# Performance work log

Measured on AMD Instinct MI355X. Metric: run time of the kernel, lower is better.

The kernel has to match this reference:

```python
import jax, jax.numpy as jnp
import numpy as np

WH = 7          # window height
WW = 7          # window width
HEADS = 8
HEAD_DIM = 64   # inner_dim = heads * 64 hard-coded in module
SCALE = HEAD_DIM ** (-0.5)


def _relative_position_index():
    # identical construction to the torch module, done once in numpy
    coords = np.stack(np.meshgrid(np.arange(WH), np.arange(WW), indexing='ij'))  # [2,Wh,Ww]
    cf = coords.reshape(2, -1)                       # [2, Wh*Ww]
    rel = cf[:, :, None] - cf[:, None, :]            # [2, N, N]
    rel = rel.transpose(1, 2, 0).copy()              # [N, N, 2]
    rel[:, :, 0] += WH - 1
    rel[:, :, 1] += WW - 1
    rel[:, :, 0] *= 2 * WW - 1
    return rel.sum(-1)                               # [N, N] int

REL_IDX = jnp.asarray(_relative_position_index())


def setup_inputs() -> dict:
    key = jax.random.key(0)
    ks = jax.random.split(key, 4)
    B, C, H, W = 32, 384, 56, 56
    inner = HEADS * HEAD_DIM  # 512
    return {
        'x': jax.random.normal(ks[0], (B, C, H, W), jnp.float32),
        'w_qkv': jax.random.normal(ks[1], (C, 3 * inner), jnp.float32) * 0.02,
        'b_qkv': jnp.zeros((3 * inner,), jnp.float32),
        'w_out': jax.random.normal(ks[2], (inner, C), jnp.float32) * 0.02,
        'b_out': jnp.zeros((C,), jnp.float32),
        'bias_table': jax.random.normal(ks[3], ((2 * WH - 1) * (2 * WW - 1), HEADS), jnp.float32) * 0.01,
    }


def reference(x, w_qkv, b_qkv, w_out, b_out, bias_table):
    B, C, H, W = x.shape
    r1, r2 = H // WH, W // WW
    N = WH * WW  # 49 tokens per window
    # window partition: b c (r1 h1) (r2 w1) -> (b r1 r2) (h1 w1) c
    xw = x.reshape(B, C, r1, WH, r2, WW).transpose(0, 2, 4, 3, 5, 1)
    xw = xw.reshape(B * r1 * r2, N, C)
    # qkv projection
    qkv = xw @ w_qkv + b_qkv                                # [BM, N, 3*inner]
    q, k, v = jnp.split(qkv, 3, axis=2)
    q = q * SCALE
    def to_heads(t):
        BM = t.shape[0]
        return t.reshape(BM, N, HEADS, HEAD_DIM).transpose(0, 2, 1, 3)  # [BM,h,N,d]
    q, k, v = to_heads(q), to_heads(k), to_heads(v)
    attn = jnp.einsum('bhmc,bhnc->bhmn', q, k)              # [BM,h,N,N]
    # relative position bias gather
    bias = bias_table[REL_IDX.reshape(-1)].reshape(N, N, HEADS).transpose(2, 0, 1)
    attn = attn + bias[None]
    attn = jax.nn.softmax(attn, axis=3)
    out = jnp.einsum('bhmn,bhnc->bhmc', attn, v)            # [BM,h,N,d]
    out = out.transpose(0, 2, 1, 3).reshape(B * r1 * r2, N, HEADS * HEAD_DIM)
    out = out @ w_out + b_out                               # [BM,N,C]
    # reverse window partition: (b r1 r2) (h1 w1) c -> b c (r1 h1) (r2 w1)
    out = out.reshape(B, r1, r2, WH, WW, C).transpose(0, 5, 1, 3, 2, 4)
    out = out.reshape(B, C, H, W)
    return out, attn
```

## Files before the change

### kernel.cpp

```cpp
#include <hip/hip_runtime.h>

typedef __attribute__((ext_vector_type(8))) short s16x8;
typedef __attribute__((ext_vector_type(4))) short s16x4;
typedef __attribute__((ext_vector_type(4))) float f32x4;

#define NTOK 49
#define CDIM 384
#define INNER 512
#define XW_STRIDE 408
#define PL_STRIDE 88

__device__ __forceinline__ short f2bf(float f) {
  unsigned u = __float_as_uint(f);
  u += 0x7fffu + ((u >> 16) & 1u);
  return (short)(u >> 16);
}

__device__ __forceinline__ f32x4 mfma16(s16x8 a, s16x8 b, f32x4 c) {
  return __builtin_amdgcn_mfma_f32_16x16x32_bf16(a, b, c, 0, 0, 0);
}

__global__ void prep_kernel(const float* __restrict__ w_qkv, const float* __restrict__ w_out,
                            const float* __restrict__ bias_table,
                            short* __restrict__ wqkvT, short* __restrict__ woutT,
                            float* __restrict__ biasm) {
  int i = blockIdx.x * 256 + threadIdx.x;
  if (i < 1536 * CDIM) {
    int col = i % 1536, k = i / 1536;
    wqkvT[(size_t)col * CDIM + k] = f2bf(w_qkv[(size_t)k * 1536 + col]);
  } else if (i < 1536 * CDIM + CDIM * INNER) {
    int j = i - 1536 * CDIM;
    int c = j % CDIM, ii = j / CDIM;
    woutT[(size_t)c * INNER + ii] = f2bf(w_out[(size_t)ii * CDIM + c]);
  } else if (i < 1536 * CDIM + CDIM * INNER + 8 * NTOK * NTOK) {
    int j = i - 1536 * CDIM - CDIM * INNER;
    int h = j / 2401, t = j % 2401;
    int m = t / 49, n = t % 49;
    int rel = (m / 7 - n / 7 + 6) * 13 + (m % 7 - n % 7 + 6);
    biasm[j] = bias_table[rel * 8 + h];
  }
}

__global__ __launch_bounds__(512, 1) void qkv_kernel(
    const float* __restrict__ x, const float* __restrict__ b_qkv,
    const short* __restrict__ wqkvT,
    short* __restrict__ qs, short* __restrict__ ks, short* __restrict__ vs) {
  __shared__ short xw[64 * XW_STRIDE];
  const int win = blockIdx.x;
  const int b = win >> 6, r1 = (win >> 3) & 7, r2 = win & 7;
  const int tid = threadIdx.x;
  const float* xb = x + (size_t)b * CDIM * 3136 + (r1 * 7) * 56 + (r2 * 7);
  {
    const int mm = tid & 63;
    const int c0 = tid >> 6;
    int xoff = -1;
    if (mm < NTOK) xoff = (mm / 7) * 56 + (mm % 7);
    for (int it = 0; it < 48; ++it) {
      int c = c0 + it * 8;
      float v = (xoff >= 0) ? xb[(size_t)c * 3136 + xoff] : 0.f;
      xw[mm * XW_STRIDE + c] = f2bf(v);
    }
  }
  __syncthreads();
  const int wave = tid >> 6, lane = tid & 63;
  const int l15 = lane & 15, l4 = lane >> 4;
  const size_t hb = (size_t)win * 8 + wave;
  for (int tile = 0; tile < 3; ++tile) {
    f32x4 acc[4][4];
#pragma unroll
    for (int fm = 0; fm < 4; ++fm)
#pragma unroll
      for (int fn = 0; fn < 4; ++fn) acc[fm][fn] = (f32x4){0.f, 0.f, 0.f, 0.f};
    const short* wb = wqkvT + ((size_t)tile * 512 + wave * 64) * CDIM;
    for (int kk = 0; kk < 12; ++kk) {
      s16x8 av[4], bv[4];
#pragma unroll
      for (int fm = 0; fm < 4; ++fm)
        av[fm] = *(const s16x8*)(&xw[(fm * 16 + l15) * XW_STRIDE + kk * 32 + l4 * 8]);
#pragma unroll
      for (int fn = 0; fn < 4; ++fn)
        bv[fn] = *(const s16x8*)(wb + (size_t)(fn * 16 + l15) * CDIM + kk * 32 + l4 * 8);
#pragma unroll
      for (int fm = 0; fm < 4; ++fm)
#pragma unroll
        for (int fn = 0; fn < 4; ++fn)
          acc[fm][fn] = mfma16(av[fm], bv[fn], acc[fm][fn]);
    }
    float bq[4];
#pragma unroll
    for (int fn = 0; fn < 4; ++fn)
      bq[fn] = b_qkv[tile * 512 + wave * 64 + fn * 16 + l15];
    if (tile < 2) {
      short* dst = (tile == 0 ? qs : ks) + hb * (NTOK * 64);
      const float scl = (tile == 0) ? 0.125f : 1.f;
#pragma unroll
      for (int fm = 0; fm < 4; ++fm)
#pragma unroll
        for (int j = 0; j < 4; ++j) {
          int m = fm * 16 + l4 * 4 + j;
          if (m < NTOK) {
#pragma unroll
            for (int fn = 0; fn < 4; ++fn)
              dst[m * 64 + fn * 16 + l15] = f2bf((acc[fm][fn][j] + bq[fn]) * scl);
          }
        }
    } else {
      short* dst = vs + hb * 4096;
#pragma unroll
      for (int fm = 0; fm < 4; ++fm) {
        int bm = fm * 16 + l4 * 4;
#pragma unroll
        for (int fn = 0; fn < 4; ++fn) {
          int d = fn * 16 + l15;
          if (bm + 3 < NTOK) {
            s16x4 pk;
#pragma unroll
            for (int j = 0; j < 4; ++j) pk[j] = f2bf(acc[fm][fn][j] + bq[fn]);
            *(s16x4*)(dst + d * 64 + bm) = pk;
          } else if (bm < NTOK) {
#pragma unroll
            for (int j = 0; j < 4; ++j)
              if (bm + j < NTOK) dst[d * 64 + bm + j] = f2bf(acc[fm][fn][j] + bq[fn]);
          }
        }
      }
    }
  }
}

__global__ __launch_bounds__(64) void attn_kernel(
    const short* __restrict__ qs, const short* __restrict__ ks, const short* __restrict__ vs,
    const float* __restrict__ biasm, float* __restrict__ attn_out, short* __restrict__ os) {
  __shared__ short pl[64 * PL_STRIDE];
  const int blk = blockIdx.x;
  const int win = blk >> 3, h = blk & 7;
  const int lane = threadIdx.x;
  const int l15 = lane & 15, l4 = lane >> 4;
  const short* qb = qs + (size_t)blk * (NTOK * 64);
  const short* kb = ks + (size_t)blk * (NTOK * 64);
  f32x4 acc[4][4];
#pragma unroll
  for (int fm = 0; fm < 4; ++fm)
#pragma unroll
    for (int fn = 0; fn < 4; ++fn) acc[fm][fn] = (f32x4){0.f, 0.f, 0.f, 0.f};
#pragma unroll
  for (int kk = 0; kk < 2; ++kk) {
    s16x8 av[4], bv[4];
#pragma unroll
    for (int fm = 0; fm < 4; ++fm)
      av[fm] = *(const s16x8*)(qb + (fm * 16 + l15) * 64 + kk * 32 + l4 * 8);
#pragma unroll
    for (int fn = 0; fn < 4; ++fn)
      bv[fn] = *(const s16x8*)(kb + (fn * 16 + l15) * 64 + kk * 32 + l4 * 8);
#pragma unroll
    for (int fm = 0; fm < 4; ++fm)
#pragma unroll
      for (int fn = 0; fn < 4; ++fn)
        acc[fm][fn] = mfma16(av[fm], bv[fn], acc[fm][fn]);
  }
  const float* bh = biasm + h * 2401;
  float* ao = attn_out + (size_t)blk * (NTOK * NTOK);
#pragma unroll
  for (int fm = 0; fm < 4; ++fm) {
#pragma unroll
    for (int j = 0; j < 4; ++j) {
      const int m = fm * 16 + l4 * 4 + j;
      const bool mok = (m < NTOK);
      float sv[4], p[4];
#pragma unroll
      for (int fn = 0; fn < 4; ++fn) {
        int n = fn * 16 + l15;
        float bias = (mok && n < NTOK) ? bh[m * 49 + n] : 0.f;
        sv[fn] = acc[fm][fn][j] + bias;
      }
      float mx = -1e30f;
#pragma unroll
      for (int fn = 0; fn < 4; ++fn)
        if (fn * 16 + l15 < NTOK) mx = fmaxf(mx, sv[fn]);
      mx = fmaxf(mx, __shfl_xor(mx, 1));
      mx = fmaxf(mx, __shfl_xor(mx, 2));
      mx = fmaxf(mx, __shfl_xor(mx, 4));
      mx = fmaxf(mx, __shfl_xor(mx, 8));
      float sum = 0.f;
#pragma unroll
      for (int fn = 0; fn < 4; ++fn) {
        int n = fn * 16 + l15;
        p[fn] = (n < NTOK) ? __expf(sv[fn] - mx) : 0.f;
        sum += p[fn];
      }
      sum += __shfl_xor(sum, 1);
      sum += __shfl_xor(sum, 2);
      sum += __shfl_xor(sum, 4);
      sum += __shfl_xor(sum, 8);
      const float inv = 1.f / sum;
#pragma unroll
      for (int fn = 0; fn < 4; ++fn) {
        int n = fn * 16 + l15;
        float pv = p[fn] * inv;
        if (mok && n < NTOK) ao[m * 49 + n] = pv;
        pl[m * PL_STRIDE + n] = f2bf(pv);
      }
    }
  }
  __syncthreads();
  const short* vb = vs + (size_t)blk * 4096;
  f32x4 oacc[4][4];
#pragma unroll
  for (int fm = 0; fm < 4; ++fm)
#pragma unroll
    for (int fn = 0; fn < 4; ++fn) oacc[fm][fn] = (f32x4){0.f, 0.f, 0.f, 0.f};
#pragma unroll
  for (int kk = 0; kk < 2; ++kk) {
    s16x8 av[4], bv[4];
#pragma unroll
    for (int fm = 0; fm < 4; ++fm)
      av[fm] = *(const s16x8*)(&pl[(fm * 16 + l15) * PL_STRIDE + kk * 32 + l4 * 8]);
#pragma unroll
    for (int fn = 0; fn < 4; ++fn)
      bv[fn] = *(const s16x8*)(vb + (fn * 16 + l15) * 64 + kk * 32 + l4 * 8);
#pragma unroll
    for (int fm = 0; fm < 4; ++fm)
#pragma unroll
      for (int fn = 0; fn < 4; ++fn)
        oacc[fm][fn] = mfma16(av[fm], bv[fn], oacc[fm][fn]);
  }
  short* ob = os + (size_t)win * (NTOK * INNER) + h * 64;
#pragma unroll
  for (int fm = 0; fm < 4; ++fm)
#pragma unroll
    for (int j = 0; j < 4; ++j) {
      int m = fm * 16 + l4 * 4 + j;
      if (m < NTOK) {
#pragma unroll
        for (int fn = 0; fn < 4; ++fn)
          ob[m * INNER + fn * 16 + l15] = f2bf(oacc[fm][fn][j]);
      }
    }
}

__global__ __launch_bounds__(384, 1) void oproj_kernel(
    const short* __restrict__ os, const short* __restrict__ woutT,
    const float* __restrict__ b_out, float* __restrict__ outp) {
  __shared__ float ot[CDIM * 57];
  const int win = blockIdx.x;
  const int b = win >> 6, r1 = (win >> 3) & 7, r2 = win & 7;
  const int tid = threadIdx.x;
  const int wave = tid >> 6, lane = tid & 63;
  const int l15 = lane & 15, l4 = lane >> 4;
  const short* ab = os + (size_t)win * (NTOK * INNER);
  const short* bb = woutT + (size_t)wave * 64 * INNER;
  f32x4 acc[4][4];
#pragma unroll
  for (int fm = 0; fm < 4; ++fm)
#pragma unroll
    for (int fn = 0; fn < 4; ++fn) acc[fm][fn] = (f32x4){0.f, 0.f, 0.f, 0.f};
  for (int kk = 0; kk < 16; ++kk) {
    s16x8 av[4], bv[4];
#pragma unroll
    for (int fm = 0; fm < 4; ++fm)
      av[fm] = *(const s16x8*)(ab + (size_t)(fm * 16 + l15) * INNER + kk * 32 + l4 * 8);
#pragma unroll
    for (int fn = 0; fn < 4; ++fn)
      bv[fn] = *(const s16x8*)(bb + (size_t)(fn * 16 + l15) * INNER + kk * 32 + l4 * 8);
#pragma unroll
    for (int fm = 0; fm < 4; ++fm)
#pragma unroll
      for (int fn = 0; fn < 4; ++fn)
        acc[fm][fn] = mfma16(av[fm], bv[fn], acc[fm][fn]);
  }
  float bo[4];
#pragma unroll
  for (int fn = 0; fn < 4; ++fn) bo[fn] = b_out[wave * 64 + fn * 16 + l15];
#pragma unroll
  for (int fm = 0; fm < 4; ++fm)
#pragma unroll
    for (int j = 0; j < 4; ++j) {
      int m = fm * 16 + l4 * 4 + j;
      if (m < NTOK) {
#pragma unroll
        for (int fn = 0; fn < 4; ++fn)
          ot[(wave * 64 + fn * 16 + l15) * 57 + m] = acc[fm][fn][j] + bo[fn];
      }
    }
  __syncthreads();
  float* ob = outp + ((size_t)b * CDIM) * 3136 + (r1 * 7) * 56 + (r2 * 7);
  for (int i = tid; i < CDIM * 7; i += 384) {
    int c = i % CDIM;
    int h1 = i / CDIM;
    float* dst = ob + (size_t)c * 3136 + h1 * 56;
    const float* src = &ot[c * 57 + h1 * 7];
#pragma unroll
    for (int w1 = 0; w1 < 7; ++w1) dst[w1] = src[w1];
  }
}

extern "C" void kernel_launch(void* const* d_in, const int* in_sizes, int n_in,
                              void* d_out, int out_size, void* d_ws, size_t ws_size,
                              hipStream_t stream) {
  const float* x          = (const float*)d_in[0];
  const float* w_qkv      = (const float*)d_in[1];
  const float* b_qkv      = (const float*)d_in[2];
  const float* w_out      = (const float*)d_in[3];
  const float* b_out      = (const float*)d_in[4];
  const float* bias_table = (const float*)d_in[5];

  const size_t NEED = 239075328ull + 102760448ull + 32768ull;
  if (ws_size < NEED) return;

  char* ws = (char*)d_ws;
  short* wqkvT = (short*)(ws + 0);
  short* woutT = (short*)(ws + 1179648);
  float* biasm = (float*)(ws + 1572864);
  short* ks    = (short*)(ws + 2097152);
  short* vs    = (short*)(ws + 104857600);
  short* os    = (short*)(ws + 239075328);

  float* outp = (float*)d_out;
  float* attn = outp + (size_t)32 * CDIM * 3136;
  short* qs   = (short*)outp;

  prep_kernel<<<3148, 256, 0, stream>>>(w_qkv, w_out, bias_table, wqkvT, woutT, biasm);
  qkv_kernel<<<2048, 512, 0, stream>>>(x, b_qkv, wqkvT, qs, ks, vs);
  attn_kernel<<<16384, 64, 0, stream>>>(qs, ks, vs, biasm, attn, os);
  oproj_kernel<<<2048, 384, 0, stream>>>(os, woutT, b_out, outp);
}
```

Baseline: 1.333 ms.

## Retile QKV projection over raw pixel rows and transpose V in attention kernel

The QKV GEMM now treats rows as 128 contiguous image pixels per channel (coalesced x loads) instead of one padded 49-token window per block. This removes the 64/49 padding waste and the strided window gather. Each block computes one of Q, K or V with 128x512 tiles and scatters results into per-window, per-head layout, with an XCD-aware block remap. V is now stored token-major without padding, and the attention kernel transposes it through LDS before the PV MMA. Costs are scattered 2-byte output stores in the projection and an extra LDS transpose per attention block.

```diff
diff --git a/kernel.cpp b/kernel.cpp
--- a/kernel.cpp
+++ b/kernel.cpp
@@ -7,8 +7,9 @@
 #define NTOK 49
 #define CDIM 384
 #define INNER 512
-#define XW_STRIDE 408
 #define PL_STRIDE 88
+#define XS_STRIDE 392
+#define VT_STRIDE 72
 
 __device__ __forceinline__ short f2bf(float f) {
   unsigned u = __float_as_uint(f);
@@ -41,88 +42,75 @@
   }
 }
 
-__global__ __launch_bounds__(512, 1) void qkv_kernel(
+__global__ __launch_bounds__(512, 2) void qkv2_kernel(
     const float* __restrict__ x, const float* __restrict__ b_qkv,
     const short* __restrict__ wqkvT,
     short* __restrict__ qs, short* __restrict__ ks, short* __restrict__ vs) {
-  __shared__ short xw[64 * XW_STRIDE];
-  const int win = blockIdx.x;
-  const int b = win >> 6, r1 = (win >> 3) & 7, r2 = win & 7;
+  __shared__ short xs[128 * XS_STRIDE];
+  const int bid = blockIdx.x;
+  const int logical = (bid & 7) * 294 + (bid >> 3);
+  const int nb = logical % 3;
+  const int mb = logical / 3;
+  const int m0 = mb * 128;
   const int tid = threadIdx.x;
-  const float* xb = x + (size_t)b * CDIM * 3136 + (r1 * 7) * 56 + (r2 * 7);
+
   {
-    const int mm = tid & 63;
-    const int c0 = tid >> 6;
-    int xoff = -1;
-    if (mm < NTOK) xoff = (mm / 7) * 56 + (mm % 7);
-    for (int it = 0; it < 48; ++it) {
-      int c = c0 + it * 8;
-      float v = (xoff >= 0) ? xb[(size_t)c * 3136 + xoff] : 0.f;
-      xw[mm * XW_STRIDE + c] = f2bf(v);
+    const int r = tid & 127, c0 = tid >> 7;
+    const int mrow = m0 + r;
+    const int g = mrow / 392, p = mrow - g * 392;
+    const float* xr = x + (size_t)(g >> 3) * (CDIM * 3136) + (g & 7) * 392 + p;
+    short* drow = &xs[r * XS_STRIDE];
+#pragma unroll 8
+    for (int it = 0; it < 96; ++it) {
+      int c = c0 + it * 4;
+      drow[c] = f2bf(xr[(size_t)c * 3136]);
     }
   }
   __syncthreads();
+
   const int wave = tid >> 6, lane = tid & 63;
   const int l15 = lane & 15, l4 = lane >> 4;
-  const size_t hb = (size_t)win * 8 + wave;
-  for (int tile = 0; tile < 3; ++tile) {
-    f32x4 acc[4][4];
-#pragma unroll
-    for (int fm = 0; fm < 4; ++fm)
-#pragma unroll
-      for (int fn = 0; fn < 4; ++fn) acc[fm][fn] = (f32x4){0.f, 0.f, 0.f, 0.f};
-    const short* wb = wqkvT + ((size_t)tile * 512 + wave * 64) * CDIM;
-    for (int kk = 0; kk < 12; ++kk) {
-      s16x8 av[4], bv[4];
+  const int wr = wave >> 2, wc = wave & 3;
+  f32x4 acc[4][8];
+#pragma unroll
+  for (int fm = 0; fm < 4; ++fm)
+#pragma unroll
+    for (int fn = 0; fn < 8; ++fn) acc[fm][fn] = (f32x4){0.f, 0.f, 0.f, 0.f};
+
+  const short* wbase = wqkvT + ((size_t)nb * 512 + wc * 128 + l15) * CDIM;
+  for (int kk = 0; kk < 12; ++kk) {
+    s16x8 av[4];
+#pragma unroll
+    for (int fm = 0; fm < 4; ++fm)
+      av[fm] = *(const s16x8*)&xs[(wr * 64 + fm * 16 + l15) * XS_STRIDE + kk * 32 + l4 * 8];
+#pragma unroll
+    for (int fn = 0; fn < 8; ++fn) {
+      s16x8 bv = *(const s16x8*)(wbase + (size_t)fn * 16 * CDIM + kk * 32 + l4 * 8);
 #pragma unroll
       for (int fm = 0; fm < 4; ++fm)
-        av[fm] = *(const s16x8*)(&xw[(fm * 16 + l15) * XW_STRIDE + kk * 32 + l4 * 8]);
-#pragma unroll
-      for (int fn = 0; fn < 4; ++fn)
-        bv[fn] = *(const s16x8*)(wb + (size_t)(fn * 16 + l15) * CDIM + kk * 32 + l4 * 8);
-#pragma unroll
-      for (int fm = 0; fm < 4; ++fm)
-#pragma unroll
-        for (int fn = 0; fn < 4; ++fn)
-          acc[fm][fn] = mfma16(av[fm], bv[fn], acc[fm][fn]);
-    }
-    float bq[4];
-#pragma unroll
-    for (int fn = 0; fn < 4; ++fn)
-      bq[fn] = b_qkv[tile * 512 + wave * 64 + fn * 16 + l15];
-    if (tile < 2) {
-      short* dst = (tile == 0 ? qs : ks) + hb * (NTOK * 64);
-      const float scl = (tile == 0) ? 0.125f : 1.f;
-#pragma unroll
-      for (int fm = 0; fm < 4; ++fm)
-#pragma unroll
-        for (int j = 0; j < 4; ++j) {
-          int m = fm * 16 + l4 * 4 + j;
-          if (m < NTOK) {
-#pragma unroll
-            for (int fn = 0; fn < 4; ++fn)
-              dst[m * 64 + fn * 16 + l15] = f2bf((acc[fm][fn][j] + bq[fn]) * scl);
-          }
-        }
-    } else {
-      short* dst = vs + hb * 4096;
-#pragma unroll
-      for (int fm = 0; fm < 4; ++fm) {
-        int bm = fm * 16 + l4 * 4;
-#pragma unroll
-        for (int fn = 0; fn < 4; ++fn) {
-          int d = fn * 16 + l15;
-          if (bm + 3 < NTOK) {
-            s16x4 pk;
-#pragma unroll
-            for (int j = 0; j < 4; ++j) pk[j] = f2bf(acc[fm][fn][j] + bq[fn]);
-            *(s16x4*)(dst + d * 64 + bm) = pk;
-          } else if (bm < NTOK) {
-#pragma unroll
-            for (int j = 0; j < 4; ++j)
-              if (bm + j < NTOK) dst[d * 64 + bm + j] = f2bf(acc[fm][fn][j] + bq[fn]);
-          }
-        }
+        acc[fm][fn] = mfma16(av[fm], bv, acc[fm][fn]);
+    }
+  }
+
+  float bq[8];
+#pragma unroll
+  for (int fn = 0; fn < 8; ++fn) bq[fn] = b_qkv[nb * 512 + wc * 128 + fn * 16 + l15];
+  const float scl = (nb == 0) ? 0.125f : 1.f;
+  short* dstt = (nb == 0) ? qs : (nb == 1 ? ks : vs);
+#pragma unroll
+  for (int fm = 0; fm < 4; ++fm) {
+#pragma unroll
+    for (int j = 0; j < 4; ++j) {
+      const int mrow = m0 + wr * 64 + fm * 16 + l4 * 4 + j;
+      const int g = mrow / 392, p = mrow - g * 392;
+      const int h1 = p / 56, xcol = p - h1 * 56;
+      const int r2 = xcol / 7, w1 = xcol - r2 * 7;
+      const size_t rowbase = (size_t)((g * 8 + r2) * 8) * 3136 + (h1 * 7 + w1) * 64;
+#pragma unroll
+      for (int fn = 0; fn < 8; ++fn) {
+        const int h = wc * 2 + (fn >> 2);
+        const int d = ((fn & 3) << 4) + l15;
+        dstt[rowbase + (size_t)h * 3136 + d] = f2bf((acc[fm][fn][j] + bq[fn]) * scl);
       }
     }
   }
@@ -132,12 +120,20 @@
     const short* __restrict__ qs, const short* __restrict__ ks, const short* __restrict__ vs,
     const float* __restrict__ biasm, float* __restrict__ attn_out, short* __restrict__ os) {
   __shared__ short pl[64 * PL_STRIDE];
+  __shared__ short vT[64 * VT_STRIDE];
   const int blk = blockIdx.x;
   const int win = blk >> 3, h = blk & 7;
   const int lane = threadIdx.x;
   const int l15 = lane & 15, l4 = lane >> 4;
   const short* qb = qs + (size_t)blk * (NTOK * 64);
   const short* kb = ks + (size_t)blk * (NTOK * 64);
+  const short* vb = vs + (size_t)blk * (NTOK * 64);
+  {
+    short* vrow = &vT[lane * VT_STRIDE];
+    for (int t = 0; t < NTOK; ++t) vrow[t] = vb[t * 64 + lane];
+#pragma unroll
+    for (int t = NTOK; t < 64; ++t) vrow[t] = 0;
+  }
   f32x4 acc[4][4];
 #pragma unroll
   for (int fm = 0; fm < 4; ++fm)
@@ -203,7 +199,6 @@
     }
   }
   __syncthreads();
-  const short* vb = vs + (size_t)blk * 4096;
   f32x4 oacc[4][4];
 #pragma unroll
   for (int fm = 0; fm < 4; ++fm)
@@ -217,7 +212,7 @@
       av[fm] = *(const s16x8*)(&pl[(fm * 16 + l15) * PL_STRIDE + kk * 32 + l4 * 8]);
 #pragma unroll
     for (int fn = 0; fn < 4; ++fn)
-      bv[fn] = *(const s16x8*)(vb + (fn * 16 + l15) * 64 + kk * 32 + l4 * 8);
+      bv[fn] = *(const s16x8*)(&vT[(fn * 16 + l15) * VT_STRIDE + kk * 32 + l4 * 8]);
 #pragma unroll
     for (int fm = 0; fm < 4; ++fm)
 #pragma unroll
@@ -304,7 +299,7 @@
   const float* b_out      = (const float*)d_in[4];
   const float* bias_table = (const float*)d_in[5];
 
-  const size_t NEED = 239075328ull + 102760448ull + 32768ull;
+  const size_t NEED = 207618048ull + 102760448ull + 32768ull;
   if (ws_size < NEED) return;
 
   char* ws = (char*)d_ws;
@@ -313,14 +308,14 @@
   float* biasm = (float*)(ws + 1572864);
   short* ks    = (short*)(ws + 2097152);
   short* vs    = (short*)(ws + 104857600);
-  short* os    = (short*)(ws + 239075328);
+  short* os    = (short*)(ws + 207618048);
 
   float* outp = (float*)d_out;
   float* attn = outp + (size_t)32 * CDIM * 3136;
   short* qs   = (short*)outp;
 
   prep_kernel<<<3148, 256, 0, stream>>>(w_qkv, w_out, bias_table, wqkvT, woutT, biasm);
-  qkv_kernel<<<2048, 512, 0, stream>>>(x, b_qkv, wqkvT, qs, ks, vs);
+  qkv2_kernel<<<2352, 512, 0, stream>>>(x, b_qkv, wqkvT, qs, ks, vs);
   attn_kernel<<<16384, 64, 0, stream>>>(qs, ks, vs, biasm, attn, os);
   oproj_kernel<<<2048, 384, 0, stream>>>(os, woutT, b_out, outp);
 }
```

New measurement: 1.161 ms. 12.9% less time.
